# Kernel optimization log

Hardware: AMD Instinct MI355X
Metric: run time of the kernel (lower is better)

Reference implementation:

```python
import jax, jax.numpy as jnp
import numpy as np

N_NODES = 50000
N_EDGES = 800000
IN_DIM = 128
HID = 96
ATTN_HID = 32
OUT_DIM = 16
N_SPOTS = 5000
EPS = 1e-5


def _glorot(k, shape):
    fan_in, fan_out = shape
    lim = float(np.sqrt(6.0 / (fan_in + fan_out)))
    return jax.random.uniform(k, shape, minval=-lim, maxval=lim, dtype=jnp.float32)


def setup_inputs() -> dict:
    key = jax.random.key(0)
    ks = jax.random.split(key, 16)
    f32 = jnp.float32
    inp = {
        'x': jax.random.normal(ks[0], (N_NODES, IN_DIM), dtype=f32),
        'edge_index': jax.random.randint(ks[1], (2, N_EDGES), 0, N_NODES, dtype=jnp.int32),
        'cell_to_spot': jax.random.randint(ks[2], (N_NODES,), 0, N_SPOTS, dtype=jnp.int32),
        'num_spots': N_SPOTS,
        # proj: Linear(IN_DIM, HID) + GraphNorm(HID)
        'proj_W': _glorot(ks[3], (IN_DIM, HID)), 'proj_b': jnp.zeros((HID,), f32),
        'gn0_w': jnp.ones((HID,), f32), 'gn0_b': jnp.zeros((HID,), f32), 'gn0_a': jnp.ones((HID,), f32),
        # GCN layer 1 + GraphNorm
        'gcn1_W': _glorot(ks[4], (HID, HID)), 'gcn1_b': jnp.zeros((HID,), f32),
        'gn1_w': jnp.ones((HID,), f32), 'gn1_b': jnp.zeros((HID,), f32), 'gn1_a': jnp.ones((HID,), f32),
        # GCN layer 2 + GraphNorm
        'gcn2_W': _glorot(ks[5], (HID, HID)), 'gcn2_b': jnp.zeros((HID,), f32),
        'gn2_w': jnp.ones((HID,), f32), 'gn2_b': jnp.zeros((HID,), f32), 'gn2_a': jnp.ones((HID,), f32),
        # spot attention aggregator MLP
        'attn_W1': _glorot(ks[6], (HID, ATTN_HID)), 'attn_b1': jnp.zeros((ATTN_HID,), f32),
        'attn_W2': _glorot(ks[7], (ATTN_HID, 1)), 'attn_b2': jnp.zeros((1,), f32),
        # MLP head: Linear + GraphNorm + ReLU + Linear
        'mlp_W1': _glorot(ks[8], (HID, HID)), 'mlp_b1': jnp.zeros((HID,), f32),
        'mlp_gn_w': jnp.ones((HID,), f32), 'mlp_gn_b': jnp.zeros((HID,), f32), 'mlp_gn_a': jnp.ones((HID,), f32),
        'mlp_W2': _glorot(ks[9], (HID, OUT_DIM)), 'mlp_b2': jnp.zeros((OUT_DIM,), f32),
    }
    return inp


def graph_norm(x, w, b, a):
    # PyG GraphNorm over the single graph (all nodes)
    mean = jnp.mean(x, axis=0, keepdims=True)           # [1, d]
    centered = x - a * mean                              # [n, d]
    var = jnp.mean(centered * centered, axis=0, keepdims=True)
    return w * centered * jax.lax.rsqrt(var + EPS) + b


def gcn_conv(x, W, b, src, dst, n):
    # PyG GCNConv: add self-loops, symmetric normalization
    h = x @ W                                            # [n, d_out]
    deg = jax.ops.segment_sum(jnp.ones((src.shape[0],), x.dtype), dst, num_segments=n) + 1.0
    dinv = jax.lax.rsqrt(deg)                            # deg >= 1 due to self loops
    norm = dinv[src] * dinv[dst]                         # [E]
    agg = jax.ops.segment_sum(h[src] * norm[:, None], dst, num_segments=n)
    agg = agg + (dinv * dinv)[:, None] * h               # self-loop messages
    return agg + b


def segment_softmax(scores, seg, num_segments):
    smax = jax.ops.segment_max(scores, seg, num_segments=num_segments)
    e = jnp.exp(scores - smax[seg])
    denom = jax.ops.segment_sum(e, seg, num_segments=num_segments)
    return e / denom[seg]


def reference(x, edge_index, cell_to_spot, num_spots,
              proj_W, proj_b, gn0_w, gn0_b, gn0_a,
              gcn1_W, gcn1_b, gn1_w, gn1_b, gn1_a,
              gcn2_W, gcn2_b, gn2_w, gn2_b, gn2_a,
              attn_W1, attn_b1, attn_W2, attn_b2,
              mlp_W1, mlp_b1, mlp_gn_w, mlp_gn_b, mlp_gn_a,
              mlp_W2, mlp_b2):
    n = x.shape[0]
    src, dst = edge_index[0], edge_index[1]
    # proj: Linear + GraphNorm + ReLU
    h = jax.nn.relu(graph_norm(x @ proj_W + proj_b, gn0_w, gn0_b, gn0_a))
    # GCN stack
    h = jax.nn.relu(graph_norm(gcn_conv(h, gcn1_W, gcn1_b, src, dst, n), gn1_w, gn1_b, gn1_a))
    h = jax.nn.relu(graph_norm(gcn_conv(h, gcn2_W, gcn2_b, src, dst, n), gn2_w, gn2_b, gn2_a))
    # spot attention aggregation
    scores = (jax.nn.relu(h @ attn_W1 + attn_b1) @ attn_W2 + attn_b2)[:, 0]  # [n]
    attn = segment_softmax(scores, cell_to_spot, num_spots)                  # [n]
    spot = jax.ops.segment_sum(h * attn[:, None], cell_to_spot, num_segments=num_spots)  # [S, d]
    # MLP head
    z = jax.nn.relu(graph_norm(spot @ mlp_W1 + mlp_b1, mlp_gn_w, mlp_gn_b, mlp_gn_a))
    return z @ mlp_W2 + mlp_b2
```

## Files before the change

kernel.cpp:

```cpp
#include <hip/hip_runtime.h>

#define N_NODES 50000
#define N_EDGES 800000
#define IN_DIM 128
#define HID 96
#define ATTN_HID 32
#define OUT_DIM 16
#define N_SPOTS 5000
#define GN_EPS 1e-5f

#define SCAN_NB ((N_NODES + 255) / 256)
#define SCAN_SB ((N_SPOTS + 255) / 256)
#define NXCD 8
#define NRANGE (N_NODES / NXCD)
#define SRANGE (N_SPOTS / NXCD)
#define CSB 256

__device__ __align__(16) float g_bufA[N_NODES * HID];
__device__ __align__(16) float g_bufB[N_NODES * HID];
__device__ __align__(16) float g_bufC[N_NODES * HID];
__device__ __align__(16) float g_spot[N_SPOTS * HID];
__device__ float    g_dinv[N_NODES];
__device__ float    g_scores[N_NODES];
__device__ int      g_deg[N_NODES];
__device__ int      g_degs[N_SPOTS];
__device__ int      g_rp[N_NODES + 1];
__device__ int      g_cur[N_NODES];
__device__ int      g_rps[N_SPOTS + 1];
__device__ int      g_curs[N_SPOTS];
__device__ int      g_csrc[N_EDGES];
__device__ int      g_cnode[N_NODES];
__device__ int      g_partN[SCAN_NB];
__device__ int      g_partS[SCAN_SB];
__device__ float    g_Spart[CSB][2 * HID];
__device__ float    g_ab[4 * 2 * HID];

__device__ __forceinline__ float* pick(int id) {
  switch (id) {
    case 0:  return g_bufA;
    case 1:  return g_bufB;
    case 2:  return g_bufC;
    default: return g_spot;
  }
}

__global__ __launch_bounds__(256) void k_init() {
  int i = blockIdx.x * 256 + threadIdx.x;
  if (i < N_NODES) g_deg[i] = 0;
  if (i < N_SPOTS) g_degs[i] = 0;
}

__global__ __launch_bounds__(256) void k_hist(const int* __restrict__ dst,
                                              const int* __restrict__ c2s) {
  int r = blockIdx.x & 7;
  int cb = blockIdx.x >> 3;
  int stride = (gridDim.x >> 3) * 256;
  int nlo = r * NRANGE, nhi = nlo + NRANGE;
  int slo = r * SRANGE, shi = slo + SRANGE;
  for (int i = cb * 256 + threadIdx.x; i < N_EDGES; i += stride) {
    int d = dst[i];
    if (d >= nlo && d < nhi) atomicAdd(&g_deg[d], 1);
  }
  for (int i = cb * 256 + threadIdx.x; i < N_NODES; i += stride) {
    int sp = c2s[i];
    if (sp >= slo && sp < shi) atomicAdd(&g_degs[sp], 1);
  }
}

__global__ __launch_bounds__(256) void k_scan1() {
  bool isS = blockIdx.x >= SCAN_NB;
  int b = isS ? blockIdx.x - SCAN_NB : blockIdx.x;
  const int n = isS ? N_SPOTS : N_NODES;
  const int* deg = isS ? g_degs : g_deg;
  int i = b * 256 + threadIdx.x;
  int v = (i < n) ? deg[i] : 0;
#pragma unroll
  for (int o = 32; o >= 1; o >>= 1) v += __shfl_xor(v, o);
  __shared__ int red[4];
  if ((threadIdx.x & 63) == 0) red[threadIdx.x >> 6] = v;
  __syncthreads();
  if (threadIdx.x == 0)
    (isS ? g_partS : g_partN)[b] = red[0] + red[1] + red[2] + red[3];
}

__global__ __launch_bounds__(256) void k_scan2() {
  bool isS = blockIdx.x == 1;
  int cnt = isS ? SCAN_SB : SCAN_NB;
  int* part = isS ? g_partS : g_partN;
  __shared__ int tmp[256];
  int t = threadIdx.x;
  int v = (t < cnt) ? part[t] : 0;
  tmp[t] = v;
  __syncthreads();
  for (int o = 1; o < 256; o <<= 1) {
    int u = (t >= o) ? tmp[t - o] : 0;
    __syncthreads();
    tmp[t] += u;
    __syncthreads();
  }
  if (t < cnt) part[t] = tmp[t] - v;
}

__global__ __launch_bounds__(256) void k_scan3() {
  bool isS = blockIdx.x >= SCAN_NB;
  int b = isS ? blockIdx.x - SCAN_NB : blockIdx.x;
  const int n = isS ? N_SPOTS : N_NODES;
  const int* deg = isS ? g_degs : g_deg;
  int* rp  = isS ? g_rps  : g_rp;
  int* cur = isS ? g_curs : g_cur;
  const int* part = isS ? g_partS : g_partN;
  __shared__ int tmp[256];
  int t = threadIdx.x;
  int i = b * 256 + t;
  int v = (i < n) ? deg[i] : 0;
  tmp[t] = v;
  __syncthreads();
  for (int o = 1; o < 256; o <<= 1) {
    int u = (t >= o) ? tmp[t - o] : 0;
    __syncthreads();
    tmp[t] += u;
    __syncthreads();
  }
  if (i < n) {
    int off = part[b] + tmp[t] - v;
    rp[i] = off;
    cur[i] = off;
    if (i == n - 1) rp[n] = off + v;
    if (!isS) g_dinv[i] = rsqrtf((float)(v + 1));
  }
}

__global__ __launch_bounds__(256) void k_fill(const int* __restrict__ src,
                                              const int* __restrict__ dst,
                                              const int* __restrict__ c2s) {
  int r = blockIdx.x & 7;
  int cb = blockIdx.x >> 3;
  int stride = (gridDim.x >> 3) * 256;
  int nlo = r * NRANGE, nhi = nlo + NRANGE;
  int slo = r * SRANGE, shi = slo + SRANGE;
  for (int i = cb * 256 + threadIdx.x; i < N_EDGES; i += stride) {
    int d = dst[i];
    if (d >= nlo && d < nhi) {
      int p = atomicAdd(&g_cur[d], 1);
      g_csrc[p] = src[i];
    }
  }
  for (int i = cb * 256 + threadIdx.x; i < N_NODES; i += stride) {
    int sp = c2s[i];
    if (sp >= slo && sp < shi) {
      int p = atomicAdd(&g_curs[sp], 1);
      g_cnode[p] = i;
    }
  }
}

template <int K, bool AFF, bool SCALE>
__global__ __launch_bounds__(256) void k_gemm96(const float* __restrict__ Aext,
                                                int a_id, int out_id,
                                                const float* __restrict__ W,
                                                const float* __restrict__ bias,
                                                int stage, int nrows) {
  constexpr int KC = 32;
  constexpr int ROWS = 64;
  __shared__ __align__(16) float Ws[KC][HID];
  __shared__ float xs[ROWS][KC + 1];
  __shared__ float abs_[2 * HID];
  const float* A = Aext ? Aext : pick(a_id);
  float* out = pick(out_id);
  int tid = threadIdx.x;
  if (AFF && tid < 2 * HID) abs_[tid] = g_ab[stage * 2 * HID + tid];
  int r0 = blockIdx.x * ROWS;
  int rg = tid >> 3;
  int cg = (tid & 7) * 12;
  float acc[2][12];
#pragma unroll
  for (int i = 0; i < 2; ++i)
#pragma unroll
    for (int c = 0; c < 12; ++c) acc[i][c] = 0.f;

  for (int k0 = 0; k0 < K; k0 += KC) {
    __syncthreads();
    for (int f = tid; f < KC * HID / 4; f += 256) {
      reinterpret_cast<float4*>(&Ws[0][0])[f] =
          reinterpret_cast<const float4*>(W + (size_t)k0 * HID)[f];
    }
    for (int f = tid; f < ROWS * KC / 4; f += 256) {
      int r = f >> 3;
      int kk = (f & 7) << 2;
      int row = r0 + r;
      float4 v = make_float4(0.f, 0.f, 0.f, 0.f);
      if (row < nrows)
        v = *reinterpret_cast<const float4*>(A + (size_t)row * K + k0 + kk);
      if (AFF) {
        int c = k0 + kk;
        v.x = fmaxf(v.x * abs_[c]     + abs_[HID + c],     0.f);
        v.y = fmaxf(v.y * abs_[c + 1] + abs_[HID + c + 1], 0.f);
        v.z = fmaxf(v.z * abs_[c + 2] + abs_[HID + c + 2], 0.f);
        v.w = fmaxf(v.w * abs_[c + 3] + abs_[HID + c + 3], 0.f);
      }
      xs[r][kk] = v.x; xs[r][kk + 1] = v.y; xs[r][kk + 2] = v.z; xs[r][kk + 3] = v.w;
    }
    __syncthreads();
#pragma unroll
    for (int k = 0; k < KC; ++k) {
      float x0 = xs[rg][k];
      float x1 = xs[rg + 32][k];
#pragma unroll
      for (int c = 0; c < 12; ++c) {
        float wv = Ws[k][cg + c];
        acc[0][c] += x0 * wv;
        acc[1][c] += x1 * wv;
      }
    }
  }
#pragma unroll
  for (int i = 0; i < 2; ++i) {
    int row = r0 + rg + 32 * i;
    if (row < nrows) {
      float sc = SCALE ? g_dinv[row] : 1.f;
#pragma unroll
      for (int c = 0; c < 12; ++c) {
        float v = acc[i][c] * sc;
        if (bias) v += bias[cg + c];
        out[(size_t)row * HID + cg + c] = v;
      }
    }
  }
}

__global__ __launch_bounds__(256) void k_gather(int t_id, const float* __restrict__ b,
                                                int agg_id) {
  const float* __restrict__ t = pick(t_id);
  float* __restrict__ agg = pick(agg_id);
  int g = (blockIdx.x * 256 + threadIdx.x) >> 5;
  int lane = threadIdx.x & 31;
  if (g >= N_NODES) return;
  int beg = g_rp[g], end = g_rp[g + 1];
  const float* __restrict__ tg = t + (size_t)g * HID;
  float a0 = tg[lane], a1 = tg[32 + lane], a2 = tg[64 + lane];
  int e = beg;
  for (; e + 8 <= end; e += 8) {
    const float* p0 = t + (size_t)g_csrc[e]     * HID;
    const float* p1 = t + (size_t)g_csrc[e + 1] * HID;
    const float* p2 = t + (size_t)g_csrc[e + 2] * HID;
    const float* p3 = t + (size_t)g_csrc[e + 3] * HID;
    const float* p4 = t + (size_t)g_csrc[e + 4] * HID;
    const float* p5 = t + (size_t)g_csrc[e + 5] * HID;
    const float* p6 = t + (size_t)g_csrc[e + 6] * HID;
    const float* p7 = t + (size_t)g_csrc[e + 7] * HID;
    a0 += p0[lane]; a1 += p0[32 + lane]; a2 += p0[64 + lane];
    a0 += p1[lane]; a1 += p1[32 + lane]; a2 += p1[64 + lane];
    a0 += p2[lane]; a1 += p2[32 + lane]; a2 += p2[64 + lane];
    a0 += p3[lane]; a1 += p3[32 + lane]; a2 += p3[64 + lane];
    a0 += p4[lane]; a1 += p4[32 + lane]; a2 += p4[64 + lane];
    a0 += p5[lane]; a1 += p5[32 + lane]; a2 += p5[64 + lane];
    a0 += p6[lane]; a1 += p6[32 + lane]; a2 += p6[64 + lane];
    a0 += p7[lane]; a1 += p7[32 + lane]; a2 += p7[64 + lane];
  }
  for (; e < end; ++e) {
    const float* __restrict__ ts = t + (size_t)g_csrc[e] * HID;
    a0 += ts[lane]; a1 += ts[32 + lane]; a2 += ts[64 + lane];
  }
  float di = g_dinv[g];
  size_t o = (size_t)g * HID;
  agg[o + lane]      = di * a0 + b[lane];
  agg[o + 32 + lane] = di * a1 + b[32 + lane];
  agg[o + 64 + lane] = di * a2 + b[64 + lane];
}

__global__ __launch_bounds__(256) void k_colstats(int x_id, int nrows) {
  const float4* __restrict__ x4 = reinterpret_cast<const float4*>(pick(x_id));
  int tid = threadIdx.x;
  bool active = tid < 240;
  int c4 = tid % 24, rs = tid / 24;
  float s1[4] = {0.f, 0.f, 0.f, 0.f}, s2[4] = {0.f, 0.f, 0.f, 0.f};
  if (active) {
    for (int r = blockIdx.x * 10 + rs; r < nrows; r += gridDim.x * 10) {
      float4 v = x4[(size_t)r * 24 + c4];
      s1[0] += v.x; s2[0] += v.x * v.x;
      s1[1] += v.y; s2[1] += v.y * v.y;
      s1[2] += v.z; s2[2] += v.z * v.z;
      s1[3] += v.w; s2[3] += v.w * v.w;
    }
  }
  __shared__ float lds1[10][HID], lds2[10][HID];
  if (active) {
#pragma unroll
    for (int j = 0; j < 4; ++j) {
      lds1[rs][c4 * 4 + j] = s1[j];
      lds2[rs][c4 * 4 + j] = s2[j];
    }
  }
  __syncthreads();
  if (tid < 2 * HID) {
    float s = 0.f;
    if (tid < HID) {
#pragma unroll
      for (int k = 0; k < 10; ++k) s += lds1[k][tid];
    } else {
#pragma unroll
      for (int k = 0; k < 10; ++k) s += lds2[k][tid - HID];
    }
    g_Spart[blockIdx.x][tid] = s;
  }
}

__global__ __launch_bounds__(256) void k_gnreduce(int stage,
                                                  const float* __restrict__ w,
                                                  const float* __restrict__ b,
                                                  const float* __restrict__ a,
                                                  float invn) {
  __shared__ float S[2 * HID];
  int tid = threadIdx.x;
  if (tid < 2 * HID) {
    float s0 = 0.f, s1 = 0.f, s2 = 0.f, s3 = 0.f;
    for (int k = 0; k < CSB; k += 4) {
      s0 += g_Spart[k][tid];
      s1 += g_Spart[k + 1][tid];
      s2 += g_Spart[k + 2][tid];
      s3 += g_Spart[k + 3][tid];
    }
    S[tid] = (s0 + s1) + (s2 + s3);
  }
  __syncthreads();
  if (tid < HID) {
    float mean = S[tid] * invn;
    float var = S[HID + tid] * invn + mean * mean * (a[tid] * a[tid] - 2.f * a[tid]);
    float r = rsqrtf(var + GN_EPS);
    float alpha = w[tid] * r;
    float* ab = g_ab + stage * 2 * HID;
    ab[tid] = alpha;
    ab[HID + tid] = b[tid] - alpha * a[tid] * mean;
  }
}

__global__ __launch_bounds__(256) void k_scores(int h_id, int stage,
                                                const float* __restrict__ W1,
                                                const float* __restrict__ b1,
                                                const float* __restrict__ W2,
                                                const float* __restrict__ b2) {
  __shared__ float W1s[HID * ATTN_HID];
  __shared__ float b1s[ATTN_HID], W2s[ATTN_HID];
  __shared__ float abs_[2 * HID];
  const float* h = pick(h_id);
  const float* ab = g_ab + stage * 2 * HID;
  int tid = threadIdx.x;
  for (int f = tid; f < HID * ATTN_HID; f += 256) W1s[f] = W1[f];
  if (tid < ATTN_HID) { b1s[tid] = b1[tid]; W2s[tid] = W2[tid]; }
  if (tid < 2 * HID) abs_[tid] = ab[tid];
  __syncthreads();
  int i = blockIdx.x * 256 + tid;
  if (i >= N_NODES) return;
  float acc[ATTN_HID];
#pragma unroll
  for (int k = 0; k < ATTN_HID; ++k) acc[k] = 0.f;
  const float4* h4 = reinterpret_cast<const float4*>(h + (size_t)i * HID);
  for (int j4 = 0; j4 < HID / 4; ++j4) {
    float4 hv4 = h4[j4];
    int j = j4 * 4;
    float h0 = fmaxf(hv4.x * abs_[j]     + abs_[HID + j],     0.f);
    float h1 = fmaxf(hv4.y * abs_[j + 1] + abs_[HID + j + 1], 0.f);
    float h2 = fmaxf(hv4.z * abs_[j + 2] + abs_[HID + j + 2], 0.f);
    float h3 = fmaxf(hv4.w * abs_[j + 3] + abs_[HID + j + 3], 0.f);
#pragma unroll
    for (int k = 0; k < ATTN_HID; ++k) {
      acc[k] += h0 * W1s[j * ATTN_HID + k] + h1 * W1s[(j + 1) * ATTN_HID + k] +
                h2 * W1s[(j + 2) * ATTN_HID + k] + h3 * W1s[(j + 3) * ATTN_HID + k];
    }
  }
  float s = b2[0];
#pragma unroll
  for (int k = 0; k < ATTN_HID; ++k) s += fmaxf(acc[k] + b1s[k], 0.f) * W2s[k];
  g_scores[i] = s;
}

__global__ __launch_bounds__(256) void k_spotagg(int h_id, int stage) {
  const float* __restrict__ h = pick(h_id);
  const float* ab = g_ab + stage * 2 * HID;
  int g = (blockIdx.x * 256 + threadIdx.x) >> 5;
  int lane = threadIdx.x & 31;
  if (g >= N_SPOTS) return;
  int beg = g_rps[g], end = g_rps[g + 1];
  float m = -1e30f;
  for (int i = beg + lane; i < end; i += 32) m = fmaxf(m, g_scores[g_cnode[i]]);
#pragma unroll
  for (int o = 16; o >= 1; o >>= 1) m = fmaxf(m, __shfl_xor(m, o, 32));
  float al0 = ab[lane],      be0 = ab[HID + lane];
  float al1 = ab[32 + lane], be1 = ab[HID + 32 + lane];
  float al2 = ab[64 + lane], be2 = ab[HID + 64 + lane];
  float a0 = 0.f, a1 = 0.f, a2 = 0.f, denom = 0.f;
  for (int i = beg; i < end; ++i) {
    int nd = g_cnode[i];
    float e = __expf(g_scores[nd] - m);
    denom += e;
    const float* __restrict__ hr = h + (size_t)nd * HID;
    a0 += e * fmaxf(hr[lane] * al0 + be0, 0.f);
    a1 += e * fmaxf(hr[32 + lane] * al1 + be1, 0.f);
    a2 += e * fmaxf(hr[64 + lane] * al2 + be2, 0.f);
  }
  float inv = (denom > 0.f) ? 1.f / denom : 0.f;
  g_spot[g * HID + lane]      = a0 * inv;
  g_spot[g * HID + 32 + lane] = a1 * inv;
  g_spot[g * HID + 64 + lane] = a2 * inv;
}

__global__ __launch_bounds__(256) void k_final(int t3_id, int stage,
                                               const float* __restrict__ W2,
                                               const float* __restrict__ b2,
                                               float* __restrict__ out) {
  __shared__ float W2s[HID * OUT_DIM];
  const float* t3 = pick(t3_id);
  const float* ab = g_ab + stage * 2 * HID;
  int tid = threadIdx.x;
  for (int f = tid; f < HID * OUT_DIM; f += 256) W2s[f] = W2[f];
  __syncthreads();
  int r = blockIdx.x * 16 + (tid >> 4);
  int c = tid & 15;
  if (r >= N_SPOTS) return;
  float acc = b2[c];
  for (int j = 0; j < HID; ++j) {
    float z = fmaxf(t3[(size_t)r * HID + j] * ab[j] + ab[HID + j], 0.f);
    acc += z * W2s[j * OUT_DIM + c];
  }
  out[r * OUT_DIM + c] = acc;
}

extern "C" void kernel_launch(void* const* d_in, const int* in_sizes, int n_in,
                              void* d_out, int out_size, void* d_ws, size_t ws_size,
                              hipStream_t stream) {
  const float* x       = (const float*)d_in[0];
  const int*   ei      = (const int*)d_in[1];
  const int*   src     = ei;
  const int*   dst     = ei + N_EDGES;
  const int*   c2s     = (const int*)d_in[2];
  const float* proj_W  = (const float*)d_in[4];
  const float* proj_b  = (const float*)d_in[5];
  const float* gn0_w   = (const float*)d_in[6];
  const float* gn0_b   = (const float*)d_in[7];
  const float* gn0_a   = (const float*)d_in[8];
  const float* gcn1_W  = (const float*)d_in[9];
  const float* gcn1_b  = (const float*)d_in[10];
  const float* gn1_w   = (const float*)d_in[11];
  const float* gn1_b   = (const float*)d_in[12];
  const float* gn1_a   = (const float*)d_in[13];
  const float* gcn2_W  = (const float*)d_in[14];
  const float* gcn2_b  = (const float*)d_in[15];
  const float* gn2_w   = (const float*)d_in[16];
  const float* gn2_b   = (const float*)d_in[17];
  const float* gn2_a   = (const float*)d_in[18];
  const float* attn_W1 = (const float*)d_in[19];
  const float* attn_b1 = (const float*)d_in[20];
  const float* attn_W2 = (const float*)d_in[21];
  const float* attn_b2 = (const float*)d_in[22];
  const float* mlp_W1  = (const float*)d_in[23];
  const float* mlp_b1  = (const float*)d_in[24];
  const float* mlp_gn_w = (const float*)d_in[25];
  const float* mlp_gn_b = (const float*)d_in[26];
  const float* mlp_gn_a = (const float*)d_in[27];
  const float* mlp_W2  = (const float*)d_in[28];
  const float* mlp_b2  = (const float*)d_in[29];
  float* out = (float*)d_out;

  const float invN = 1.f / (float)N_NODES;
  const float invS = 1.f / (float)N_SPOTS;
  const int GB_N = (N_NODES + 63) / 64;
  const int GB_S = (N_SPOTS + 63) / 64;
  const int XB   = NXCD * 96;
  const int GTH  = (N_NODES * 32 + 255) / 256;
  const int SPB  = (N_SPOTS * 32 + 255) / 256;
  const int SCB  = SCAN_NB + SCAN_SB;

  k_init<<<(N_NODES + 255) / 256, 256, 0, stream>>>();
  k_hist<<<XB, 256, 0, stream>>>(dst, c2s);
  k_scan1<<<SCB, 256, 0, stream>>>();
  k_scan2<<<2, 256, 0, stream>>>();
  k_scan3<<<SCB, 256, 0, stream>>>();
  k_fill<<<XB, 256, 0, stream>>>(src, dst, c2s);

  k_gemm96<IN_DIM, false, false><<<GB_N, 256, 0, stream>>>(x, -1, 0, proj_W, proj_b, 0, N_NODES);
  k_colstats<<<CSB, 256, 0, stream>>>(0, N_NODES);
  k_gnreduce<<<1, 256, 0, stream>>>(0, gn0_w, gn0_b, gn0_a, invN);

  k_gemm96<HID, true, true><<<GB_N, 256, 0, stream>>>(nullptr, 0, 1, gcn1_W, nullptr, 0, N_NODES);
  k_gather<<<GTH, 256, 0, stream>>>(1, gcn1_b, 0);
  k_colstats<<<CSB, 256, 0, stream>>>(0, N_NODES);
  k_gnreduce<<<1, 256, 0, stream>>>(1, gn1_w, gn1_b, gn1_a, invN);

  k_gemm96<HID, true, true><<<GB_N, 256, 0, stream>>>(nullptr, 0, 2, gcn2_W, nullptr, 1, N_NODES);
  k_gather<<<GTH, 256, 0, stream>>>(2, gcn2_b, 1);
  k_colstats<<<CSB, 256, 0, stream>>>(1, N_NODES);
  k_gnreduce<<<1, 256, 0, stream>>>(2, gn2_w, gn2_b, gn2_a, invN);

  k_scores<<<(N_NODES + 255) / 256, 256, 0, stream>>>(1, 2, attn_W1, attn_b1, attn_W2, attn_b2);
  k_spotagg<<<SPB, 256, 0, stream>>>(1, 2);

  k_gemm96<HID, false, false><<<GB_S, 256, 0, stream>>>(nullptr, 3, 2, mlp_W1, mlp_b1, 0, N_SPOTS);
  k_colstats<<<CSB, 256, 0, stream>>>(2, N_SPOTS);
  k_gnreduce<<<1, 256, 0, stream>>>(3, mlp_gn_w, mlp_gn_b, mlp_gn_a, invS);
  k_final<<<(N_SPOTS + 15) / 16, 256, 0, stream>>>(2, 3, mlp_W2, mlp_b2, out);
}
```

Before: 435.4 us.

## Use split-bf16 MFMA for node GEMMs and fuse column stats into gather

Replaces the scalar fp32 GEMM kernels for the projection and both GCN layers with an MFMA kernel. It uses a three-product split-bf16 scheme (hi*hi + hi*lo + lo*hi) to approximate fp32 accuracy on the matrix cores. The gather kernel now also computes per-block column sums and sums of squares, reduced by a small colred kernel. This removes the separate colstats pass that re-read the full node feature buffer. The fused stats add a block-wide sync and shared-memory reduction to the gather kernel, and the split-bf16 product is not bit-exact to fp32.

```diff
diff --git a/kernel.cpp b/kernel.cpp
--- a/kernel.cpp
+++ b/kernel.cpp
@@ -15,6 +15,10 @@
 #define NRANGE (N_NODES / NXCD)
 #define SRANGE (N_SPOTS / NXCD)
 #define CSB 256
+#define GTHB 6250
+
+typedef short bf16x8 __attribute__((ext_vector_type(8)));
+typedef float f32x4 __attribute__((ext_vector_type(4)));
 
 __device__ __align__(16) float g_bufA[N_NODES * HID];
 __device__ __align__(16) float g_bufB[N_NODES * HID];
@@ -32,6 +36,7 @@
 __device__ int      g_cnode[N_NODES];
 __device__ int      g_partN[SCAN_NB];
 __device__ int      g_partS[SCAN_SB];
+__device__ float    g_gpart[GTHB][2 * HID];
 __device__ float    g_Spart[CSB][2 * HID];
 __device__ float    g_ab[4 * 2 * HID];
 
@@ -42,6 +47,12 @@
     case 2:  return g_bufC;
     default: return g_spot;
   }
+}
+
+__device__ __forceinline__ unsigned short bf16_rn(float f) {
+  unsigned u = __float_as_uint(f);
+  unsigned r = u + 0x7FFFu + ((u >> 16) & 1u);
+  return (unsigned short)(r >> 16);
 }
 
 __global__ __launch_bounds__(256) void k_init() {
@@ -150,6 +161,97 @@
     if (sp >= slo && sp < shi) {
       int p = atomicAdd(&g_curs[sp], 1);
       g_cnode[p] = i;
+    }
+  }
+}
+
+template <int K, bool AFF, bool SCALE>
+__global__ __launch_bounds__(256) void k_mfma(const float* __restrict__ Aext,
+                                              int a_id, int out_id,
+                                              const float* __restrict__ W,
+                                              const float* __restrict__ bias,
+                                              int stage, int nrows) {
+  constexpr int CH = K / 32;
+  __shared__ unsigned short WF[CH][6][64][8];
+  __shared__ unsigned short WL[CH][6][64][8];
+  __shared__ float abs_[2 * HID];
+  __shared__ float bs[HID];
+  const float* A = Aext ? Aext : pick(a_id);
+  float* out = pick(out_id);
+  int tid = threadIdx.x;
+  if (AFF && tid < 2 * HID) abs_[tid] = g_ab[stage * 2 * HID + tid];
+  if (tid < HID) bs[tid] = bias ? bias[tid] : 0.f;
+  for (int idx = tid; idx < CH * 6 * 64; idx += 256) {
+    int lane = idx & 63;
+    int ct = (idx >> 6) % 6;
+    int ch = idx / (6 * 64);
+    int kbase = ch * 32 + (lane >> 4) * 8;
+    int c = ct * 16 + (lane & 15);
+#pragma unroll
+    for (int j = 0; j < 8; ++j) {
+      float w = W[(size_t)(kbase + j) * HID + c];
+      unsigned short h = bf16_rn(w);
+      WF[ch][ct][lane][j] = h;
+      WL[ch][ct][lane][j] = bf16_rn(w - __uint_as_float((unsigned)h << 16));
+    }
+  }
+  __syncthreads();
+
+  int wv = tid >> 6, lane = tid & 63;
+  int r0 = blockIdx.x * 64 + wv * 16;
+  int arow = r0 + (lane & 15);
+  f32x4 acc[6];
+#pragma unroll
+  for (int t = 0; t < 6; ++t) acc[t] = (f32x4){0.f, 0.f, 0.f, 0.f};
+
+  for (int ch = 0; ch < CH; ++ch) {
+    int ks = ch * 32 + (lane >> 4) * 8;
+    float av[8];
+    if (arow < nrows) {
+      const float4* ap = reinterpret_cast<const float4*>(A + (size_t)arow * K + ks);
+      float4 v0 = ap[0], v1 = ap[1];
+      av[0] = v0.x; av[1] = v0.y; av[2] = v0.z; av[3] = v0.w;
+      av[4] = v1.x; av[5] = v1.y; av[6] = v1.z; av[7] = v1.w;
+    } else {
+#pragma unroll
+      for (int j = 0; j < 8; ++j) av[j] = 0.f;
+    }
+    if (AFF) {
+#pragma unroll
+      for (int j = 0; j < 8; ++j)
+        av[j] = fmaxf(av[j] * abs_[ks + j] + abs_[HID + ks + j], 0.f);
+    }
+    bf16x8 ah, al;
+#pragma unroll
+    for (int j = 0; j < 8; ++j) {
+      unsigned short h = bf16_rn(av[j]);
+      ah[j] = (short)h;
+      al[j] = (short)bf16_rn(av[j] - __uint_as_float((unsigned)h << 16));
+    }
+#pragma unroll
+    for (int ct = 0; ct < 6; ++ct) {
+      bf16x8 bh = *reinterpret_cast<const bf16x8*>(&WF[ch][ct][lane][0]);
+      bf16x8 bl = *reinterpret_cast<const bf16x8*>(&WL[ch][ct][lane][0]);
+      acc[ct] = __builtin_amdgcn_mfma_f32_16x16x32_bf16(al, bh, acc[ct], 0, 0, 0);
+      acc[ct] = __builtin_amdgcn_mfma_f32_16x16x32_bf16(ah, bl, acc[ct], 0, 0, 0);
+      acc[ct] = __builtin_amdgcn_mfma_f32_16x16x32_bf16(ah, bh, acc[ct], 0, 0, 0);
+    }
+  }
+  int rbase = r0 + (lane >> 4) * 4;
+  float dv[4];
+#pragma unroll
+  for (int j = 0; j < 4; ++j) {
+    int r = rbase + j;
+    dv[j] = SCALE ? ((r < nrows) ? g_dinv[r] : 0.f) : 1.f;
+  }
+#pragma unroll
+  for (int ct = 0; ct < 6; ++ct) {
+    int col = ct * 16 + (lane & 15);
+    float bb = bs[col];
+#pragma unroll
+    for (int j = 0; j < 4; ++j) {
+      int r = rbase + j;
+      if (r < nrows) out[(size_t)r * HID + col] = acc[ct][j] * dv[j] + bb;
     }
   }
 }
@@ -234,7 +336,6 @@
   float* __restrict__ agg = pick(agg_id);
   int g = (blockIdx.x * 256 + threadIdx.x) >> 5;
   int lane = threadIdx.x & 31;
-  if (g >= N_NODES) return;
   int beg = g_rp[g], end = g_rp[g + 1];
   const float* __restrict__ tg = t + (size_t)g * HID;
   float a0 = tg[lane], a1 = tg[32 + lane], a2 = tg[64 + lane];
@@ -262,10 +363,40 @@
     a0 += ts[lane]; a1 += ts[32 + lane]; a2 += ts[64 + lane];
   }
   float di = g_dinv[g];
+  float v0 = di * a0 + b[lane];
+  float v1 = di * a1 + b[32 + lane];
+  float v2 = di * a2 + b[64 + lane];
   size_t o = (size_t)g * HID;
-  agg[o + lane]      = di * a0 + b[lane];
-  agg[o + 32 + lane] = di * a1 + b[32 + lane];
-  agg[o + 64 + lane] = di * a2 + b[64 + lane];
+  agg[o + lane]      = v0;
+  agg[o + 32 + lane] = v1;
+  agg[o + 64 + lane] = v2;
+  float q0 = v0, q1 = v1, q2 = v2;
+  float r0s = v0 * v0, r1s = v1 * v1, r2s = v2 * v2;
+  q0 += __shfl_xor(q0, 32); r0s += __shfl_xor(r0s, 32);
+  q1 += __shfl_xor(q1, 32); r1s += __shfl_xor(r1s, 32);
+  q2 += __shfl_xor(q2, 32); r2s += __shfl_xor(r2s, 32);
+  __shared__ float sred[4][32][6];
+  int wv = threadIdx.x >> 6, ln = threadIdx.x & 63;
+  if (ln < 32) {
+    sred[wv][ln][0] = q0;  sred[wv][ln][1] = r0s;
+    sred[wv][ln][2] = q1;  sred[wv][ln][3] = r1s;
+    sred[wv][ln][4] = q2;  sred[wv][ln][5] = r2s;
+  }
+  __syncthreads();
+  if (threadIdx.x < 192) {
+    int l2 = threadIdx.x / 6, j = threadIdx.x % 6;
+    float s = sred[0][l2][j] + sred[1][l2][j] + sred[2][l2][j] + sred[3][l2][j];
+    int dim = l2 + (j >> 1) * 32;
+    g_gpart[blockIdx.x][(j & 1) ? HID + dim : dim] = s;
+  }
+}
+
+__global__ __launch_bounds__(256) void k_colred(int count) {
+  int tid = threadIdx.x;
+  if (tid >= 2 * HID) return;
+  float s = 0.f;
+  for (int k = blockIdx.x; k < count; k += gridDim.x) s += g_gpart[k][tid];
+  g_Spart[blockIdx.x][tid] = s;
 }
 
 __global__ __launch_bounds__(256) void k_colstats(int x_id, int nrows) {
@@ -466,7 +597,6 @@
   const int GB_N = (N_NODES + 63) / 64;
   const int GB_S = (N_SPOTS + 63) / 64;
   const int XB   = NXCD * 96;
-  const int GTH  = (N_NODES * 32 + 255) / 256;
   const int SPB  = (N_SPOTS * 32 + 255) / 256;
   const int SCB  = SCAN_NB + SCAN_SB;
 
@@ -477,18 +607,18 @@
   k_scan3<<<SCB, 256, 0, stream>>>();
   k_fill<<<XB, 256, 0, stream>>>(src, dst, c2s);
 
-  k_gemm96<IN_DIM, false, false><<<GB_N, 256, 0, stream>>>(x, -1, 0, proj_W, proj_b, 0, N_NODES);
+  k_mfma<IN_DIM, false, false><<<GB_N, 256, 0, stream>>>(x, -1, 0, proj_W, proj_b, 0, N_NODES);
   k_colstats<<<CSB, 256, 0, stream>>>(0, N_NODES);
   k_gnreduce<<<1, 256, 0, stream>>>(0, gn0_w, gn0_b, gn0_a, invN);
 
-  k_gemm96<HID, true, true><<<GB_N, 256, 0, stream>>>(nullptr, 0, 1, gcn1_W, nullptr, 0, N_NODES);
-  k_gather<<<GTH, 256, 0, stream>>>(1, gcn1_b, 0);
-  k_colstats<<<CSB, 256, 0, stream>>>(0, N_NODES);
+  k_mfma<HID, true, true><<<GB_N, 256, 0, stream>>>(nullptr, 0, 1, gcn1_W, nullptr, 0, N_NODES);
+  k_gather<<<GTHB, 256, 0, stream>>>(1, gcn1_b, 0);
+  k_colred<<<CSB, 256, 0, stream>>>(GTHB);
   k_gnreduce<<<1, 256, 0, stream>>>(1, gn1_w, gn1_b, gn1_a, invN);
 
-  k_gemm96<HID, true, true><<<GB_N, 256, 0, stream>>>(nullptr, 0, 2, gcn2_W, nullptr, 1, N_NODES);
-  k_gather<<<GTH, 256, 0, stream>>>(2, gcn2_b, 1);
-  k_colstats<<<CSB, 256, 0, stream>>>(1, N_NODES);
+  k_mfma<HID, true, true><<<GB_N, 256, 0, stream>>>(nullptr, 0, 2, gcn2_W, nullptr, 1, N_NODES);
+  k_gather<<<GTHB, 256, 0, stream>>>(2, gcn2_b, 1);
+  k_colred<<<CSB, 256, 0, stream>>>(GTHB);
   k_gnreduce<<<1, 256, 0, stream>>>(2, gn2_w, gn2_b, gn2_a, invN);
 
   k_scores<<<(N_NODES + 255) / 256, 256, 0, stream>>>(1, 2, attn_W1, attn_b1, attn_W2, attn_b2);
```

After: 366.9 us. 15.7% less time.
